# Performance work log

Measured on AMD Instinct MI355X. Metric: run time of the kernel, lower is better.

Reference implementation:

```python
import jax, jax.numpy as jnp
import numpy as np
from jax import lax

N = 50000
E = 320000
IN_DIM = 128
OUT_DIM = 64
N_CHANNEL = 8
KERNEL = 3
N_REL = 500
BN_EPS = 1e-5


def setup_inputs() -> dict:
    key = jax.random.key(0)
    ks = jax.random.split(key, 10)
    inp = jax.random.normal(ks[0], (N, IN_DIM), dtype=jnp.float32)
    heads = jax.random.randint(ks[1], (E,), 0, N)
    rels = jax.random.randint(ks[2], (E,), 0, N_REL)
    tails = jax.random.randint(ks[3], (E,), 0, N)
    triple = jnp.stack([heads, rels, tails], axis=1).astype(jnp.int64)
    # parameters
    limit_W = float(np.sqrt(6.0 / (IN_DIM + OUT_DIM)))  # xavier_uniform
    W = jax.random.uniform(ks[4], (IN_DIM, OUT_DIM), minval=-limit_W, maxval=limit_W, dtype=jnp.float32)
    rel_embed = jax.random.normal(ks[5], (N_REL, OUT_DIM), dtype=jnp.float32)
    fan_in = 1 * KERNEL * KERNEL
    b = float(1.0 / np.sqrt(fan_in))
    conv_w = jax.random.uniform(ks[6], (N_CHANNEL, 1, KERNEL, KERNEL), minval=-b, maxval=b, dtype=jnp.float32)
    conv_b = jax.random.uniform(ks[7], (N_CHANNEL,), minval=-b, maxval=b, dtype=jnp.float32)
    fc_in = N_CHANNEL * (OUT_DIM - KERNEL + 1) * (3 - KERNEL + 1)
    bf = float(1.0 / np.sqrt(fc_in))
    fc_w = jax.random.uniform(ks[8], (1, fc_in), minval=-bf, maxval=bf, dtype=jnp.float32)
    bn1_gamma = jnp.ones((1,), jnp.float32)
    bn1_beta = jnp.zeros((1,), jnp.float32)
    bn2_gamma = jnp.ones((N_CHANNEL,), jnp.float32)
    bn2_beta = jnp.zeros((N_CHANNEL,), jnp.float32)
    return {"input": inp, "triple": triple, "W": W, "rel_embed": rel_embed,
            "conv_w": conv_w, "conv_b": conv_b, "fc_w": fc_w,
            "bn1_gamma": bn1_gamma, "bn1_beta": bn1_beta,
            "bn2_gamma": bn2_gamma, "bn2_beta": bn2_beta}


def _bn_eval(x, gamma, beta):
    # eval-mode BatchNorm with running_mean=0, running_var=1
    scale = gamma / jnp.sqrt(1.0 + BN_EPS)
    return x * scale.reshape(1, -1, 1, 1) + beta.reshape(1, -1, 1, 1)


def reference(input, triple, W, rel_embed, conv_w, conv_b, fc_w,
              bn1_gamma, bn1_beta, bn2_gamma, bn2_beta):
    n = input.shape[0]
    inp = input @ W                       # [N, out_dim]
    head = triple[:, 0]
    tail = triple[:, 2]
    h = inp[head]                         # [E, D]
    r = rel_embed[triple[:, 1]]           # [E, D]
    t = inp[tail]                         # [E, D]
    # energy function: [E,1,D,3] -> bn1 -> conv -> bn2 -> relu -> fc
    x = jnp.stack([h, r, t], axis=-1)[:, None, :, :]   # [E,1,D,3]
    x = _bn_eval(x, bn1_gamma, bn1_beta)
    y = lax.conv_general_dilated(x, conv_w, (1, 1), 'VALID',
                                 dimension_numbers=('NCHW', 'OIHW', 'NCHW'))
    y = y + conv_b.reshape(1, -1, 1, 1)                 # [E,C,D-2,1]
    y = jax.nn.relu(_bn_eval(y, bn2_gamma, bn2_beta))
    y = y.reshape(y.shape[0], -1)
    e = y @ fc_w[0]                                     # [E]
    e = jax.nn.leaky_relu(e, 0.01)
    # sparse softmax over rows (head) then sparse mm with input_
    m = jax.ops.segment_max(e, head, num_segments=n)
    ex = jnp.exp(e - m[head])
    denom = jax.ops.segment_sum(ex, head, num_segments=n)
    attn = ex / denom[head]
    agg = jax.ops.segment_sum(attn[:, None] * t, head, num_segments=n)
    return jax.nn.elu(agg + inp)
```

## Files before the change

### kernel.cpp

```cpp
#include <hip/hip_runtime.h>
#include <hip/hip_bf16.h>
#include <stdint.h>

#define IN_DIM   128
#define OUT_DIM  64
#define NCH      8
#define N_REL    500
#define BN_EPS   1e-5f
#define CAP      32


#define KEEP(x) asm volatile("" : "+v"(x))

__device__ __forceinline__ float dpp_shl1(float x) {
    return __int_as_float(__builtin_amdgcn_update_dpp(
        0, __float_as_int(x), 0x130, 0xf, 0xf, true));
}

__device__ __forceinline__ void fold_cw_thread(
    const float* __restrict__ conv_w, const float* __restrict__ conv_b,
    const float* __restrict__ bn1g, const float* __restrict__ bn1b,
    const float* __restrict__ bn2g, const float* __restrict__ bn2b,
    float* __restrict__ cw, int c)
{
    if (c >= NCH) return;
    float rs  = rsqrtf(1.f + BN_EPS);
    float s1  = bn1g[0] * rs;
    float be1 = bn1b[0];
    float s2  = bn2g[c] * rs;
    float k1  = s1 * s2;
    float wsum = 0.f;
    for (int d = 0; d < 3; ++d) {
        float a  = conv_w[c * 9 + d * 3 + 0];
        float b  = conv_w[c * 9 + d * 3 + 1];
        float cc = conv_w[c * 9 + d * 3 + 2];
        wsum += a + b + cc;
        cw[c * 3 + d]      = k1 * a;
        cw[24 + c * 3 + d] = k1 * b;
        cw[48 + c * 3 + d] = k1 * cc;
    }
    cw[72 + c] = (be1 * wsum + conv_b[c]) * s2 + bn2b[c];
}

__global__ __launch_bounds__(256) void k_bucket(
    const int* __restrict__ triple,
    const float* __restrict__ conv_w, const float* __restrict__ conv_b,
    const float* __restrict__ bn1g, const float* __restrict__ bn1b,
    const float* __restrict__ bn2g, const float* __restrict__ bn2b,
    int* __restrict__ cnt, int2* __restrict__ rt32, float* __restrict__ cw,
    int E, int N)
{
    const int gtid    = blockIdx.x * 256 + threadIdx.x;
    const int gstride = gridDim.x * 256;
    if (blockIdx.x == 0 && threadIdx.x < NCH)
        fold_cw_thread(conv_w, conv_b, bn1g, bn1b, bn2g, bn2b, cw, threadIdx.x);
    for (int j = gtid; j < E; j += gstride) {
        int h = triple[3 * j], r = triple[3 * j + 1], t = triple[3 * j + 2];
        h = min(max(h, 0), N - 1);
        r = min(max(r, 0), N_REL - 1);
        t = min(max(t, 0), N - 1);
        int pos = atomicAdd(&cnt[h], 1);
        if (pos < CAP) rt32[(unsigned)h * CAP + pos] = make_int2(r, t);
    }
}

__global__ __launch_bounds__(256) void k_gemm(
    const float* __restrict__ X, const float* __restrict__ W,
    float* __restrict__ out, int N)
{
    __shared__ float Wl[IN_DIM * OUT_DIM];
    __shared__ float Xl[32 * IN_DIM];
    const int rows0 = blockIdx.x * 32;

    const float4* W4 = (const float4*)W;
    for (int i = threadIdx.x; i < IN_DIM * OUT_DIM / 4; i += 256)
        ((float4*)Wl)[i] = W4[i];
    for (int i = threadIdx.x; i < 32 * IN_DIM / 4; i += 256) {
        int r = i >> 5, k4 = i & 31;
        int rr = rows0 + r;
        float4 v = make_float4(0.f, 0.f, 0.f, 0.f);
        if (rr < N) v = ((const float4*)X)[(unsigned)rr * (IN_DIM / 4) + k4];
        ((float4*)Xl)[i] = v;
    }
    __syncthreads();

    const int w = threadIdx.x >> 6;
    const int c = threadIdx.x & 63;
    float acc[8];
    #pragma unroll
    for (int r = 0; r < 8; ++r) acc[r] = 0.f;

    for (int k4 = 0; k4 < IN_DIM / 4; ++k4) {
        int k = k4 * 4;
        float w0 = Wl[(k + 0) * OUT_DIM + c];
        float w1 = Wl[(k + 1) * OUT_DIM + c];
        float w2 = Wl[(k + 2) * OUT_DIM + c];
        float w3 = Wl[(k + 3) * OUT_DIM + c];
        #pragma unroll
        for (int r = 0; r < 8; ++r) {
            const float4 x = *(const float4*)&Xl[(w * 8 + r) * IN_DIM + k];
            acc[r] = fmaf(x.w, w3, fmaf(x.z, w2, fmaf(x.y, w1, fmaf(x.x, w0, acc[r]))));
        }
    }
    #pragma unroll
    for (int r = 0; r < 8; ++r) {
        int rr = rows0 + w * 8 + r;
        if (rr < N) out[(unsigned)rr * OUT_DIM + c] = acc[r];
    }
}

__device__ __forceinline__ float dpp_wave_sum(float x) {
    x += __int_as_float(__builtin_amdgcn_update_dpp(0, __float_as_int(x), 0x111, 0xf, 0xf, true));
    x += __int_as_float(__builtin_amdgcn_update_dpp(0, __float_as_int(x), 0x112, 0xf, 0xf, true));
    x += __int_as_float(__builtin_amdgcn_update_dpp(0, __float_as_int(x), 0x114, 0xf, 0xf, true));
    x += __int_as_float(__builtin_amdgcn_update_dpp(0, __float_as_int(x), 0x118, 0xf, 0xf, true));
    x += __int_as_float(__builtin_amdgcn_update_dpp(0, __float_as_int(x), 0x142, 0xf, 0xf, true));
    x += __int_as_float(__builtin_amdgcn_update_dpp(0, __float_as_int(x), 0x143, 0xf, 0xf, true));
    return __int_as_float(__builtin_amdgcn_readlane(__float_as_int(x), 63));
}

__global__ __launch_bounds__(256, 4) void k_fused_all(
    const float* __restrict__ inp, const float* __restrict__ rel_embed,
    const float* __restrict__ cw, const float* __restrict__ fc_w,
    const int* __restrict__ cnt, const int2* __restrict__ rt32,
    float* __restrict__ out, int N)
{
    const int lane   = threadIdx.x & 63;
    const int wave   = (blockIdx.x * (blockDim.x >> 6)) + (threadIdx.x >> 6);
    const int nwaves = gridDim.x * (blockDim.x >> 6);

    float fcl[NCH];
    #pragma unroll
    for (int c = 0; c < NCH; ++c) {
        fcl[c] = (lane < 62) ? fc_w[c * 62 + lane] : 0.f;
        KEEP(fcl[c]);
    }

    for (int h = wave; h < N; h += nwaves) {
        const int deg = min(cnt[h], CAP);

        float h0 = inp[(unsigned)h * OUT_DIM + lane];
        float h1 = dpp_shl1(h0);
        float h2 = dpp_shl1(h1);
        float Ht[NCH];
        #pragma unroll
        for (int c = 0; c < NCH; ++c) {
            float v = cw[72 + c];
            v = fmaf(cw[c * 3 + 0], h0, v);
            v = fmaf(cw[c * 3 + 1], h1, v);
            v = fmaf(cw[c * 3 + 2], h2, v);
            Ht[c] = v;
            KEEP(Ht[c]);
        }

        float m_run = -INFINITY, l_run = 0.f, agg = 0.f;
        int2 rtv = make_int2(0, 0);
        if (lane < deg) rtv = rt32[(unsigned)h * CAP + lane];

        if (deg > 0) {
            int rk = __builtin_amdgcn_readlane(rtv.x, 0);
            int tk = __builtin_amdgcn_readlane(rtv.y, 0);
            float rr = rel_embed[(unsigned)rk * OUT_DIM + lane];
            float tt = inp      [(unsigned)tk * OUT_DIM + lane];

            for (int k = 0; k < deg; ++k) {
                int rk1 = __builtin_amdgcn_readlane(rtv.x, k + 1);
                int tk1 = __builtin_amdgcn_readlane(rtv.y, k + 1);
                float rrN = rel_embed[(unsigned)rk1 * OUT_DIM + lane];
                float ttN = inp      [(unsigned)tk1 * OUT_DIM + lane];

                float r1 = dpp_shl1(rr), r2 = dpp_shl1(r1);
                float t1 = dpp_shl1(tt), t2 = dpp_shl1(t1);

                float acc = 0.f;
                #pragma unroll
                for (int c = 0; c < NCH; ++c) {
                    float y = Ht[c];
                    y = fmaf(cw[24 + c * 3 + 0], rr, y);
                    y = fmaf(cw[24 + c * 3 + 1], r1, y);
                    y = fmaf(cw[24 + c * 3 + 2], r2, y);
                    y = fmaf(cw[48 + c * 3 + 0], tt, y);
                    y = fmaf(cw[48 + c * 3 + 1], t1, y);
                    y = fmaf(cw[48 + c * 3 + 2], t2, y);
                    acc = fmaf(fmaxf(y, 0.f), fcl[c], acc);
                }
                float s  = dpp_wave_sum(acc);
                float ev = fmaxf(s, 0.01f * s);

                float mn = fmaxf(m_run, ev);
                float sc = __expf(m_run - mn);
                float wk = __expf(ev - mn);
                agg   = fmaf(agg, sc, wk * tt);
                l_run = fmaf(l_run, sc, wk);
                m_run = mn;

                rr = rrN; tt = ttN;
            }
        }
        float aggn = (l_run > 0.f) ? agg / l_run : 0.f;
        float x = aggn + h0;
        float y = x > 0.f ? x : (__expf(x) - 1.f);
        out[(unsigned)h * OUT_DIM + lane] = y;
    }
}

extern "C" void kernel_launch(void* const* d_in, const int* in_sizes, int n_in,
                              void* d_out, int out_size, void* d_ws, size_t ws_size,
                              hipStream_t stream)
{
    const float* input     = (const float*)d_in[0];
    const int*   triple    = (const int*)d_in[1];
    const float* W         = (const float*)d_in[2];
    const float* rel_embed = (const float*)d_in[3];
    const float* conv_w    = (const float*)d_in[4];
    const float* conv_b    = (const float*)d_in[5];
    const float* fc_w      = (const float*)d_in[6];
    const float* bn1g      = (const float*)d_in[7];
    const float* bn1b      = (const float*)d_in[8];
    const float* bn2g      = (const float*)d_in[9];
    const float* bn2b      = (const float*)d_in[10];
    float*       out       = (float*)d_out;

    const int N = in_sizes[0] / IN_DIM;
    const int E = in_sizes[1] / 3;

    auto align = [](size_t x) { return (x + 255) & ~(size_t)255; };
    char* base = (char*)d_ws;
    size_t o = 0;
    float* inp  = (float*)(base + o); o = align(o + (size_t)N * OUT_DIM * 4);
    int2*  rt32 = (int2*)(base + o);  o = align(o + (size_t)N * CAP * 8);
    float* cw   = (float*)(base + o); o = align(o + 80 * 4);
    int*   cnt  = (int*)(base + o);   o = align(o + (size_t)N * 4);

    hipMemsetAsync(cnt, 0, (size_t)N * 4, stream);

    k_bucket<<<(E + 255) / 256, 256, 0, stream>>>(
        triple, conv_w, conv_b, bn1g, bn1b, bn2g, bn2b, cnt, rt32, cw, E, N);
    k_gemm<<<(N + 31) / 32, 256, 0, stream>>>(input, W, inp, N);
    k_fused_all<<<4096, 256, 0, stream>>>(inp, rel_embed, cw, fc_w,
                                          cnt, rt32, out, N);
}
```

Measured before the change: 202.0 us.

## Merge bucketing and GEMM into one launch; launch one wave per node

The separate bucket and GEMM kernels become one heterogeneous launch: the first blocks do the input projection GEMM and the remaining blocks do edge bucketing plus the conv-weight folding. Independent work can then overlap and one kernel launch is saved. The fused attention kernel drops its launch-bounds occupancy hint and now runs one wave per node instead of a fixed 4096-block grid-stride loop. The merged kernel reserves the 48KB of shared memory for every block, including the bucket blocks, which may limit how many of them are resident at once.

```diff
diff --git a/kernel.cpp b/kernel.cpp
--- a/kernel.cpp
+++ b/kernel.cpp
@@ -42,70 +42,69 @@
     cw[72 + c] = (be1 * wsum + conv_b[c]) * s2 + bn2b[c];
 }
 
-__global__ __launch_bounds__(256) void k_bucket(
+__global__ __launch_bounds__(256) void k_build(
+    const float* __restrict__ X, const float* __restrict__ W,
     const int* __restrict__ triple,
     const float* __restrict__ conv_w, const float* __restrict__ conv_b,
     const float* __restrict__ bn1g, const float* __restrict__ bn1b,
     const float* __restrict__ bn2g, const float* __restrict__ bn2b,
-    int* __restrict__ cnt, int2* __restrict__ rt32, float* __restrict__ cw,
-    int E, int N)
-{
-    const int gtid    = blockIdx.x * 256 + threadIdx.x;
-    const int gstride = gridDim.x * 256;
-    if (blockIdx.x == 0 && threadIdx.x < NCH)
-        fold_cw_thread(conv_w, conv_b, bn1g, bn1b, bn2g, bn2b, cw, threadIdx.x);
-    for (int j = gtid; j < E; j += gstride) {
-        int h = triple[3 * j], r = triple[3 * j + 1], t = triple[3 * j + 2];
-        h = min(max(h, 0), N - 1);
-        r = min(max(r, 0), N_REL - 1);
-        t = min(max(t, 0), N - 1);
-        int pos = atomicAdd(&cnt[h], 1);
-        if (pos < CAP) rt32[(unsigned)h * CAP + pos] = make_int2(r, t);
-    }
-}
-
-__global__ __launch_bounds__(256) void k_gemm(
-    const float* __restrict__ X, const float* __restrict__ W,
-    float* __restrict__ out, int N)
+    float* __restrict__ inp, int* __restrict__ cnt, int2* __restrict__ rt32,
+    float* __restrict__ cw, int E, int N, int ngemm)
 {
     __shared__ float Wl[IN_DIM * OUT_DIM];
     __shared__ float Xl[32 * IN_DIM];
-    const int rows0 = blockIdx.x * 32;
-
-    const float4* W4 = (const float4*)W;
-    for (int i = threadIdx.x; i < IN_DIM * OUT_DIM / 4; i += 256)
-        ((float4*)Wl)[i] = W4[i];
-    for (int i = threadIdx.x; i < 32 * IN_DIM / 4; i += 256) {
-        int r = i >> 5, k4 = i & 31;
-        int rr = rows0 + r;
-        float4 v = make_float4(0.f, 0.f, 0.f, 0.f);
-        if (rr < N) v = ((const float4*)X)[(unsigned)rr * (IN_DIM / 4) + k4];
-        ((float4*)Xl)[i] = v;
-    }
-    __syncthreads();
-
-    const int w = threadIdx.x >> 6;
-    const int c = threadIdx.x & 63;
-    float acc[8];
-    #pragma unroll
-    for (int r = 0; r < 8; ++r) acc[r] = 0.f;
-
-    for (int k4 = 0; k4 < IN_DIM / 4; ++k4) {
-        int k = k4 * 4;
-        float w0 = Wl[(k + 0) * OUT_DIM + c];
-        float w1 = Wl[(k + 1) * OUT_DIM + c];
-        float w2 = Wl[(k + 2) * OUT_DIM + c];
-        float w3 = Wl[(k + 3) * OUT_DIM + c];
+
+    if ((int)blockIdx.x < ngemm) {
+        const int rows0 = blockIdx.x * 32;
+        const float4* W4 = (const float4*)W;
+        for (int i = threadIdx.x; i < IN_DIM * OUT_DIM / 4; i += 256)
+            ((float4*)Wl)[i] = W4[i];
+        for (int i = threadIdx.x; i < 32 * IN_DIM / 4; i += 256) {
+            int r = i >> 5, k4 = i & 31;
+            int rr = rows0 + r;
+            float4 v = make_float4(0.f, 0.f, 0.f, 0.f);
+            if (rr < N) v = ((const float4*)X)[(unsigned)rr * (IN_DIM / 4) + k4];
+            ((float4*)Xl)[i] = v;
+        }
+        __syncthreads();
+
+        const int w = threadIdx.x >> 6;
+        const int c = threadIdx.x & 63;
+        float acc[8];
+        #pragma unroll
+        for (int r = 0; r < 8; ++r) acc[r] = 0.f;
+
+        for (int k4 = 0; k4 < IN_DIM / 4; ++k4) {
+            int k = k4 * 4;
+            float w0 = Wl[(k + 0) * OUT_DIM + c];
+            float w1 = Wl[(k + 1) * OUT_DIM + c];
+            float w2 = Wl[(k + 2) * OUT_DIM + c];
+            float w3 = Wl[(k + 3) * OUT_DIM + c];
+            #pragma unroll
+            for (int r = 0; r < 8; ++r) {
+                const float4 x = *(const float4*)&Xl[(w * 8 + r) * IN_DIM + k];
+                acc[r] = fmaf(x.w, w3, fmaf(x.z, w2, fmaf(x.y, w1, fmaf(x.x, w0, acc[r]))));
+            }
+        }
         #pragma unroll
         for (int r = 0; r < 8; ++r) {
-            const float4 x = *(const float4*)&Xl[(w * 8 + r) * IN_DIM + k];
-            acc[r] = fmaf(x.w, w3, fmaf(x.z, w2, fmaf(x.y, w1, fmaf(x.x, w0, acc[r]))));
-        }
-    }
-    #pragma unroll
-    for (int r = 0; r < 8; ++r) {
-        int rr = rows0 + w * 8 + r;
-        if (rr < N) out[(unsigned)rr * OUT_DIM + c] = acc[r];
+            int rr = rows0 + w * 8 + r;
+            if (rr < N) inp[(unsigned)rr * OUT_DIM + c] = acc[r];
+        }
+    } else {
+        const int bb   = blockIdx.x - ngemm;
+        const int gtid = bb * 256 + threadIdx.x;
+        if (bb == 0 && threadIdx.x < NCH)
+            fold_cw_thread(conv_w, conv_b, bn1g, bn1b, bn2g, bn2b, cw, threadIdx.x);
+        if (gtid < E) {
+            int j = gtid;
+            int h = triple[3 * j], r = triple[3 * j + 1], t = triple[3 * j + 2];
+            h = min(max(h, 0), N - 1);
+            r = min(max(r, 0), N_REL - 1);
+            t = min(max(t, 0), N - 1);
+            int pos = atomicAdd(&cnt[h], 1);
+            if (pos < CAP) rt32[(unsigned)h * CAP + pos] = make_int2(r, t);
+        }
     }
 }
 
@@ -119,7 +118,7 @@
     return __int_as_float(__builtin_amdgcn_readlane(__float_as_int(x), 63));
 }
 
-__global__ __launch_bounds__(256, 4) void k_fused_all(
+__global__ __launch_bounds__(256) void k_fused_all(
     const float* __restrict__ inp, const float* __restrict__ rel_embed,
     const float* __restrict__ cw, const float* __restrict__ fc_w,
     const int* __restrict__ cnt, const int2* __restrict__ rt32,
@@ -234,9 +233,13 @@
 
     hipMemsetAsync(cnt, 0, (size_t)N * 4, stream);
 
-    k_bucket<<<(E + 255) / 256, 256, 0, stream>>>(
-        triple, conv_w, conv_b, bn1g, bn1b, bn2g, bn2b, cnt, rt32, cw, E, N);
-    k_gemm<<<(N + 31) / 32, 256, 0, stream>>>(input, W, inp, N);
-    k_fused_all<<<4096, 256, 0, stream>>>(inp, rel_embed, cw, fc_w,
+    const int ngemm   = (N + 31) / 32;
+    const int nbucket = (E + 255) / 256;
+    k_build<<<ngemm + nbucket, 256, 0, stream>>>(
+        input, W, triple, conv_w, conv_b, bn1g, bn1b, bn2g, bn2b,
+        inp, cnt, rt32, cw, E, N, ngemm);
+
+    const int nblk = (N + 3) / 4;
+    k_fused_all<<<nblk, 256, 0, stream>>>(inp, rel_embed, cw, fc_w,
                                           cnt, rt32, out, N);
 }
```

New measurement: 195.5 us. 3.2% less time.
